# Optimization experiments

Measured on AMD Instinct MI355X. Metric: run time of the kernel, lower is better.

Reference implementation:

```python
import jax, jax.numpy as jnp
import numpy as np

B, S, C = 4, 2048, 768
H = 6
D = C // H  # head_dim = 128


def setup_inputs() -> dict:
    key = jax.random.key(0)
    k_x, k_wa, k_ba, k_wp, k_bp = jax.random.split(key, 5)
    scale = 1.0 / np.sqrt(C)
    return {
        "x": jax.random.normal(k_x, (B, S, C), dtype=jnp.float32),
        "w_attn": jax.random.normal(k_wa, (C, 3 * C), dtype=jnp.float32) * scale,
        "b_attn": jax.random.normal(k_ba, (3 * C,), dtype=jnp.float32) * 0.02,
        "w_proj": jax.random.normal(k_wp, (C, C), dtype=jnp.float32) * scale,
        "b_proj": jax.random.normal(k_bp, (C,), dtype=jnp.float32) * 0.02,
    }


def reference(x, w_attn, b_attn, w_proj, b_proj):
    Bb, Ss, Cc = x.shape
    qkv = x @ w_attn + b_attn                      # [B,S,3C]
    q, k, v = jnp.split(qkv, 3, axis=-1)
    # [B,S,C] -> [B,H,S,D]
    q = q.reshape(Bb, Ss, H, D).transpose(0, 2, 1, 3)
    k = k.reshape(Bb, Ss, H, D).transpose(0, 2, 1, 3)
    v = v.reshape(Bb, Ss, H, D).transpose(0, 2, 1, 3)
    scores = jnp.einsum("bhsd,bhtd->bhst", q, k) / jnp.sqrt(jnp.float32(D))
    causal = jnp.tril(jnp.ones((Ss, Ss), dtype=bool))  # [S,S]
    scores = jnp.where(causal[None, None], scores, -jnp.inf)
    attn = jax.nn.softmax(scores, axis=-1)             # [B,H,S,S]
    out = jnp.einsum("bhst,bhtd->bhsd", attn, v)       # [B,H,S,D]
    out = out.transpose(0, 2, 1, 3).reshape(Bb, Ss, Cc)
    return out @ w_proj + b_proj
```

## Files before the change

kernel.cpp:

```cpp
#include <hip/hip_runtime.h>
#include <hip/hip_bf16.h>
#include <stdint.h>

#define SS 2048
#define CC 768
#define C3 2304
#define NITEMS (32 * 24)

typedef float f32x4 __attribute__((ext_vector_type(4)));
typedef short s16x8 __attribute__((ext_vector_type(8)));

__device__ __forceinline__ unsigned short f2bf(float f) {
  union { float f; unsigned int u; } v; v.f = f;
  unsigned int r = (v.u + 0x7FFFu + ((v.u >> 16) & 1u)) >> 16;
  return (unsigned short)r;
}

__device__ __forceinline__ s16x8 ld8(const unsigned short* p) {
  return *reinterpret_cast<const s16x8*>(p);
}

__device__ __forceinline__ unsigned int cvt_pk_bf16(float lo, float hi) {
  unsigned int r;
  asm("v_cvt_pk_bf16_f32 %0, %1, %2" : "=v"(r) : "v"(lo), "v"(hi));
  return r;
}

__device__ __forceinline__ void gload_lds16(const unsigned short* g, unsigned short* l) {
  __builtin_amdgcn_global_load_lds(
      (const __attribute__((address_space(1))) void*)g,
      (__attribute__((address_space(3))) void*)l, 16, 0, 0);
}

__global__ __launch_bounds__(256) void cast_bf16_kernel(
    const float* __restrict__ src, unsigned short* __restrict__ dst, int n4) {
  int i = blockIdx.x * 256 + threadIdx.x;
  if (i < n4) {
    float4 v = reinterpret_cast<const float4*>(src)[i];
    ushort4 o;
    o.x = f2bf(v.x); o.y = f2bf(v.y); o.z = f2bf(v.z); o.w = f2bf(v.w);
    reinterpret_cast<ushort4*>(dst)[i] = o;
  }
}

__global__ __launch_bounds__(256) void transpose_cast_kernel(
    const float* __restrict__ src, unsigned short* __restrict__ dst, int R, int C) {
  __shared__ float tile[32][33];
  int c0 = blockIdx.x * 32, r0 = blockIdx.y * 32;
  int tx = threadIdx.x & 31, ty = threadIdx.x >> 5;
  #pragma unroll
  for (int i = 0; i < 32; i += 8)
    tile[ty + i][tx] = src[(size_t)(r0 + ty + i) * C + c0 + tx];
  __syncthreads();
  #pragma unroll
  for (int i = 0; i < 32; i += 8)
    dst[(size_t)(c0 + ty + i) * R + r0 + tx] = f2bf(tile[tx][ty + i]);
}

__global__ __launch_bounds__(256) void vtrans_kernel(
    const unsigned short* __restrict__ qkv, unsigned short* __restrict__ vT) {
  __shared__ unsigned short t[64 * 128];
  const int tid = threadIdx.x;
  const int n0 = blockIdx.x * 64;
  const int bh = blockIdx.y;
  const int b = bh / 6, h = bh % 6;
  #pragma unroll
  for (int it = 0; it < 4; ++it) {
    int c = it * 256 + tid;
    int n = c >> 4, slot = c & 15;
    s16x8 v = ld8(qkv + (size_t)(b * SS + n0 + n) * C3 + 2 * CC + h * 128 + slot * 8);
    int ss = slot ^ ((n >> 3) & 7);
    *reinterpret_cast<s16x8*>(&t[n * 128 + ss * 8]) = v;
  }
  __syncthreads();
  #pragma unroll
  for (int it = 0; it < 4; ++it) {
    int c = it * 256 + tid;
    int d = c >> 3, n8 = (c & 7) * 8;
    s16x8 o;
    #pragma unroll
    for (int j = 0; j < 8; ++j) {
      int n = n8 + j;
      int sl = (d >> 3) ^ ((n >> 3) & 7);
      o[j] = (short)t[n * 128 + sl * 8 + (d & 7)];
    }
    *reinterpret_cast<s16x8*>(&vT[((size_t)bh * 128 + d) * SS + n0 + n8]) = o;
  }
}

template <int OUT_BF16>
__global__ __launch_bounds__(256) void gemm_lds_kernel(
    const unsigned short* __restrict__ A, const unsigned short* __restrict__ Bt,
    const float* __restrict__ bias, void* __restrict__ out, int M, int N, int K) {
  __shared__ unsigned short lA[2][128 * 32];
  __shared__ unsigned short lB[2][128 * 32];
  const int tid = threadIdx.x, lane = tid & 63, w = tid >> 6;
  const int nbx = gridDim.x;
  int bid = blockIdx.y * nbx + blockIdx.x;
  const int cpx = (nbx * gridDim.y) >> 3;
  bid = (bid & 7) * cpx + (bid >> 3);
  const int m0 = (bid / nbx) * 128, n0 = (bid % nbx) * 128;
  const int lm = lane & 15, lg = lane >> 4;
  const int wm = (w >> 1) * 64, wn = (w & 1) * 64;
  const int sr = lane >> 2;
  const int ssl = ((lane & 3) ^ ((sr >> 1) & 3)) * 8;
  int aOff[4], bOff[4];
  #pragma unroll
  for (int i = 0; i < 4; ++i) {
    int ra = wm + i * 16 + lm, rb = wn + i * 16 + lm;
    aOff[i] = ra * 32 + ((lg ^ ((ra >> 1) & 3)) * 8);
    bOff[i] = rb * 32 + ((lg ^ ((rb >> 1) & 3)) * 8);
  }
  f32x4 acc[4][4] = {};
  const int nt = K / 32;
  #pragma unroll 1
  for (int t = -1; t < nt; ++t) {
    if (t + 1 < nt) {
      const int k0 = (t + 1) * 32;
      const int cs = (t + 1) & 1;
      #pragma unroll
      for (int i = 0; i < 2; ++i) {
        int c = w * 2 + i;
        int row = c * 16 + sr;
        gload_lds16(A + (size_t)(m0 + row) * K + k0 + ssl, &lA[cs][c * 512]);
        gload_lds16(Bt + (size_t)(n0 + row) * K + k0 + ssl, &lB[cs][c * 512]);
      }
    }
    if (t >= 0) {
      const int cu = t & 1;
      s16x8 af[4], bf[4];
      #pragma unroll
      for (int i = 0; i < 4; ++i) af[i] = ld8(&lA[cu][aOff[i]]);
      #pragma unroll
      for (int i = 0; i < 4; ++i) bf[i] = ld8(&lB[cu][bOff[i]]);
      __builtin_amdgcn_s_setprio(1);
      #pragma unroll
      for (int mi = 0; mi < 4; ++mi)
        #pragma unroll
        for (int ni = 0; ni < 4; ++ni)
          acc[mi][ni] = __builtin_amdgcn_mfma_f32_16x16x32_bf16(af[mi], bf[ni], acc[mi][ni], 0, 0, 0);
      __builtin_amdgcn_s_setprio(0);
    }
    __syncthreads();
  }
  #pragma unroll
  for (int mi = 0; mi < 4; ++mi) {
    #pragma unroll
    for (int ni = 0; ni < 4; ++ni) {
      const int row = m0 + wm + mi * 16 + lg * 4;
      const int col = n0 + wn + ni * 16 + lm;
      const float bs = bias[col];
      #pragma unroll
      for (int r = 0; r < 4; ++r) {
        float v = acc[mi][ni][r] + bs;
        if (OUT_BF16)
          ((unsigned short*)out)[(size_t)(row + r) * N + col] = f2bf(v);
        else
          ((float*)out)[(size_t)(row + r) * N + col] = v;
      }
    }
  }
}

__global__ __launch_bounds__(256) void attn_kernel(
    const unsigned short* __restrict__ qkv,
    const unsigned short* __restrict__ vT,
    unsigned short* __restrict__ aout,
    int* __restrict__ ctr) {
  const int tid = threadIdx.x, lane = tid & 63, w = tid >> 6;
  const int lm = lane & 15, lg = lane >> 4;
  __shared__ unsigned short kbuf[2][64 * 128];
  __shared__ unsigned short vbuf[2][128 * 64];
  __shared__ unsigned int pb[4][16 * 44];
  __shared__ int s_item;
  const float scale = 0.08838834764831845f;
  unsigned int* pr = &pb[w][lm * 44];
  const int klg4 = lane >> 4, ks16 = lane & 15;
  const int vlg8 = lane >> 3, vs8 = lane & 7;
  for (;;) {
    __syncthreads();
    if (tid == 0) s_item = atomicAdd(ctr, 1);
    __syncthreads();
    const int item = s_item;
    if (item >= NITEMS) return;
    const int qt = 31 - (item / 24);
    const int bh = item % 24;
    const int b = bh / 6, h = bh % 6;
    const int q0 = qt * 64, wq0 = q0 + w * 16;
    const unsigned short* base = qkv + (size_t)b * SS * C3;
    const unsigned short* kg = base + CC + h * 128;
    const unsigned short* vg = vT + (size_t)bh * 128 * SS;
    s16x8 qf[4];
    {
      const unsigned short* qp = base + (size_t)(wq0 + lm) * C3 + h * 128 + lg * 8;
      #pragma unroll
      for (int ks = 0; ks < 4; ++ks) qf[ks] = ld8(qp + ks * 32);
    }
    f32x4 oacc[8] = {};
    float m_run = -1e30f, l_run = 0.0f;
    const int nt = qt + 1;
    #pragma unroll 1
    for (int t = -1; t < nt; ++t) {
      if (t + 1 < nt) {
        const int n1 = (t + 1) * 64;
        const int cs = (t + 1) & 1;
        #pragma unroll
        for (int i = 0; i < 4; ++i) {
          int c = w * 4 + i;
          int r = c * 4 + klg4;
          gload_lds16(kg + (size_t)(n1 + r) * C3 + ((ks16 ^ (r & 7)) * 8),
                      &kbuf[cs][c * 512]);
        }
        #pragma unroll
        for (int i = 0; i < 4; ++i) {
          int c = w * 4 + i;
          int d = c * 8 + vlg8;
          gload_lds16(vg + (size_t)d * SS + n1 + ((vs8 ^ vlg8) * 8),
                      &vbuf[cs][c * 512]);
        }
      }
      if (t >= 0) {
        const int n0 = t * 64;
        const int cu = t & 1;
        const unsigned short* kb = kbuf[cu];
        const unsigned short* vb = vbuf[cu];
        f32x4 sacc[4] = {};
        __builtin_amdgcn_s_setprio(1);
        #pragma unroll
        for (int nsub = 0; nsub < 4; ++nsub) {
          const int kr = (nsub * 16 + lm) * 128;
          #pragma unroll
          for (int ks = 0; ks < 4; ++ks) {
            s16x8 kf = ld8(&kb[kr + (((ks * 4 + lg) ^ (lm & 7)) * 8)]);
            sacc[nsub] = __builtin_amdgcn_mfma_f32_16x16x32_bf16(kf, qf[ks], sacc[nsub], 0, 0, 0);
          }
        }
        __builtin_amdgcn_s_setprio(0);
        const int qg = wq0 + lm;
        const bool full = (n0 + 63 <= wq0);
        float xs[4][4];
        float tmax = -1e30f;
        #pragma unroll
        for (int nsub = 0; nsub < 4; ++nsub) {
          #pragma unroll
          for (int r = 0; r < 4; ++r) {
            int n = n0 + nsub * 16 + lg * 4 + r;
            float x = sacc[nsub][r] * scale;
            if (!full && n > qg) x = -1e30f;
            xs[nsub][r] = x;
            tmax = fmaxf(tmax, x);
          }
        }
        tmax = fmaxf(tmax, __shfl_xor(tmax, 16));
        tmax = fmaxf(tmax, __shfl_xor(tmax, 32));
        const bool noresc = __all(tmax - m_run <= 8.0f);
        const float m_new = noresc ? m_run : fmaxf(m_run, tmax);
        float psum = 0.0f;
        unsigned int pk_[4][2];
        #pragma unroll
        for (int nsub = 0; nsub < 4; ++nsub) {
          float p0 = __expf(xs[nsub][0] - m_new);
          float p1 = __expf(xs[nsub][1] - m_new);
          float p2 = __expf(xs[nsub][2] - m_new);
          float p3 = __expf(xs[nsub][3] - m_new);
          psum += (p0 + p1) + (p2 + p3);
          pk_[nsub][0] = cvt_pk_bf16(p0, p1);
          pk_[nsub][1] = cvt_pk_bf16(p2, p3);
        }
        psum += __shfl_xor(psum, 16);
        psum += __shfl_xor(psum, 32);
        if (!noresc) {
          const float resc = __expf(m_run - m_new);
          l_run *= resc;
          m_run = m_new;
          float rs[4];
          #pragma unroll
          for (int r = 0; r < 4; ++r) rs[r] = __shfl(resc, lg * 4 + r);
          #pragma unroll
          for (int dsub = 0; dsub < 8; ++dsub)
            #pragma unroll
            for (int r = 0; r < 4; ++r) oacc[dsub][r] *= rs[r];
        }
        l_run += psum;
        #pragma unroll
        for (int nsub = 0; nsub < 4; ++nsub) {
          uint2 pk2; pk2.x = pk_[nsub][0]; pk2.y = pk_[nsub][1];
          *reinterpret_cast<uint2*>(&pr[nsub * 8 + lg * 2]) = pk2;
        }
        __builtin_amdgcn_s_setprio(1);
        #pragma unroll
        for (int nch = 0; nch < 2; ++nch) {
          s16x8 pf = *reinterpret_cast<const s16x8*>(&pr[nch * 16 + lg * 4]);
          #pragma unroll
          for (int dsub = 0; dsub < 8; ++dsub) {
            const int vr = (dsub * 16 + lm) * 64;
            s16x8 vf = ld8(&vb[vr + (((nch * 4 + lg) ^ (lm & 7)) * 8)]);
            oacc[dsub] = __builtin_amdgcn_mfma_f32_16x16x32_bf16(pf, vf, oacc[dsub], 0, 0, 0);
          }
        }
        __builtin_amdgcn_s_setprio(0);
      }
      __syncthreads();
    }
    float linv[4];
    #pragma unroll
    for (int r = 0; r < 4; ++r) linv[r] = 1.0f / __shfl(l_run, lg * 4 + r);
    #pragma unroll
    for (int dsub = 0; dsub < 8; ++dsub) {
      const int col = h * 128 + dsub * 16 + lm;
      #pragma unroll
      for (int r = 0; r < 4; ++r)
        aout[(size_t)(b * SS + wq0 + lg * 4 + r) * CC + col] =
            f2bf(oacc[dsub][r] * linv[r]);
    }
  }
}

extern "C" void kernel_launch(void* const* d_in, const int* in_sizes, int n_in,
                              void* d_out, int out_size, void* d_ws, size_t ws_size,
                              hipStream_t stream) {
  const float* x      = (const float*)d_in[0];
  const float* w_attn = (const float*)d_in[1];
  const float* b_attn = (const float*)d_in[2];
  const float* w_proj = (const float*)d_in[3];
  const float* b_proj = (const float*)d_in[4];
  float* out = (float*)d_out;

  const size_t M = 4 * (size_t)SS;
  unsigned short* ws = (unsigned short*)d_ws;
  unsigned short* xb   = ws;
  unsigned short* waT  = xb + M * CC;
  unsigned short* wpT  = waT + (size_t)C3 * CC;
  unsigned short* qkv  = wpT + (size_t)CC * CC;
  unsigned short* aout = qkv + M * C3;
  unsigned short* vT   = xb;
  int* ctr = (int*)(aout + M * CC);

  int n4 = (int)(M * CC / 4);
  cast_bf16_kernel<<<(n4 + 255) / 256, 256, 0, stream>>>(x, xb, n4);
  transpose_cast_kernel<<<dim3(C3 / 32, CC / 32), 256, 0, stream>>>(w_attn, waT, CC, C3);
  transpose_cast_kernel<<<dim3(CC / 32, CC / 32), 256, 0, stream>>>(w_proj, wpT, CC, CC);

  gemm_lds_kernel<1><<<dim3(C3 / 128, M / 128), 256, 0, stream>>>(
      xb, waT, b_attn, (void*)qkv, (int)M, C3, CC);

  vtrans_kernel<<<dim3(SS / 64, 24), 256, 0, stream>>>(qkv, vT);

  hipMemsetAsync(ctr, 0, sizeof(int), stream);
  attn_kernel<<<512, 256, 0, stream>>>(qkv, vT, aout, ctr);

  gemm_lds_kernel<0><<<dim3(CC / 128, M / 128), 256, 0, stream>>>(
      aout, wpT, b_proj, (void*)out, (int)M, CC, CC);
}
```

Before: 195.4 us.

## Use partial vmcnt waits so next-stage loads overlap compute in GEMM and attention

Restructures the double-buffered loops in both the GEMM and attention kernels. The first stage is now issued before the loop. Each iteration issues the next stage's global-to-LDS loads and then waits only for the older group with s_waitcnt vmcnt(N), followed by an explicit barrier. Before, __syncthreads at the end of each iteration drained every outstanding load, including the prefetch just issued, so prefetch could not overlap compute. The change depends on hand-counted vmcnt values matching the number of loads issued per stage; a wrong count would be a correctness hazard.

```diff
diff --git a/kernel.cpp b/kernel.cpp
--- a/kernel.cpp
+++ b/kernel.cpp
@@ -113,35 +113,44 @@
   }
   f32x4 acc[4][4] = {};
   const int nt = K / 32;
+  #define GSTAGE(tt, bb)                                                      \
+    {                                                                         \
+      const int k0_ = (tt) * 32;                                              \
+      _Pragma("unroll")                                                       \
+      for (int i_ = 0; i_ < 2; ++i_) {                                        \
+        int c_ = w * 2 + i_;                                                  \
+        int row_ = c_ * 16 + sr;                                              \
+        gload_lds16(A + (size_t)(m0 + row_) * K + k0_ + ssl, &lA[bb][c_ * 512]); \
+        gload_lds16(Bt + (size_t)(n0 + row_) * K + k0_ + ssl, &lB[bb][c_ * 512]); \
+      }                                                                       \
+    }
+  GSTAGE(0, 0);
   #pragma unroll 1
-  for (int t = -1; t < nt; ++t) {
+  for (int t = 0; t < nt; ++t) {
     if (t + 1 < nt) {
-      const int k0 = (t + 1) * 32;
-      const int cs = (t + 1) & 1;
-      #pragma unroll
-      for (int i = 0; i < 2; ++i) {
-        int c = w * 2 + i;
-        int row = c * 16 + sr;
-        gload_lds16(A + (size_t)(m0 + row) * K + k0 + ssl, &lA[cs][c * 512]);
-        gload_lds16(Bt + (size_t)(n0 + row) * K + k0 + ssl, &lB[cs][c * 512]);
-      }
-    }
-    if (t >= 0) {
-      const int cu = t & 1;
-      s16x8 af[4], bf[4];
-      #pragma unroll
-      for (int i = 0; i < 4; ++i) af[i] = ld8(&lA[cu][aOff[i]]);
-      #pragma unroll
-      for (int i = 0; i < 4; ++i) bf[i] = ld8(&lB[cu][bOff[i]]);
-      __builtin_amdgcn_s_setprio(1);
-      #pragma unroll
-      for (int mi = 0; mi < 4; ++mi)
-        #pragma unroll
-        for (int ni = 0; ni < 4; ++ni)
-          acc[mi][ni] = __builtin_amdgcn_mfma_f32_16x16x32_bf16(af[mi], bf[ni], acc[mi][ni], 0, 0, 0);
-      __builtin_amdgcn_s_setprio(0);
-    }
-    __syncthreads();
+      GSTAGE(t + 1, (t + 1) & 1);
+      asm volatile("s_waitcnt vmcnt(4)" ::: "memory");
+    } else {
+      asm volatile("s_waitcnt vmcnt(0)" ::: "memory");
+    }
+    __builtin_amdgcn_sched_barrier(0);
+    __builtin_amdgcn_s_barrier();
+    const int cu = t & 1;
+    s16x8 af[4], bf[4];
+    #pragma unroll
+    for (int i = 0; i < 4; ++i) af[i] = ld8(&lA[cu][aOff[i]]);
+    #pragma unroll
+    for (int i = 0; i < 4; ++i) bf[i] = ld8(&lB[cu][bOff[i]]);
+    __builtin_amdgcn_s_setprio(1);
+    #pragma unroll
+    for (int mi = 0; mi < 4; ++mi)
+      #pragma unroll
+      for (int ni = 0; ni < 4; ++ni)
+        acc[mi][ni] = __builtin_amdgcn_mfma_f32_16x16x32_bf16(af[mi], bf[ni], acc[mi][ni], 0, 0, 0);
+    __builtin_amdgcn_s_setprio(0);
+    asm volatile("s_waitcnt lgkmcnt(0)" ::: "memory");
+    __builtin_amdgcn_sched_barrier(0);
+    __builtin_amdgcn_s_barrier();
   }
   #pragma unroll
   for (int mi = 0; mi < 4; ++mi) {
@@ -160,6 +169,7 @@
       }
     }
   }
+  #undef GSTAGE
 }
 
 __global__ __launch_bounds__(256) void attn_kernel(
@@ -196,112 +206,122 @@
       #pragma unroll
       for (int ks = 0; ks < 4; ++ks) qf[ks] = ld8(qp + ks * 32);
     }
+    #define ASTAGE(tt, bb)                                                    \
+      {                                                                       \
+        const int n1_ = (tt) * 64;                                            \
+        _Pragma("unroll")                                                     \
+        for (int i_ = 0; i_ < 4; ++i_) {                                      \
+          int c_ = w * 4 + i_;                                                \
+          int r_ = c_ * 4 + klg4;                                             \
+          gload_lds16(kg + (size_t)(n1_ + r_) * C3 + ((ks16 ^ (r_ & 7)) * 8), \
+                      &kbuf[bb][c_ * 512]);                                   \
+        }                                                                     \
+        _Pragma("unroll")                                                     \
+        for (int i_ = 0; i_ < 4; ++i_) {                                      \
+          int c_ = w * 4 + i_;                                                \
+          int d_ = c_ * 8 + vlg8;                                             \
+          gload_lds16(vg + (size_t)d_ * SS + n1_ + ((vs8 ^ vlg8) * 8),        \
+                      &vbuf[bb][c_ * 512]);                                   \
+        }                                                                     \
+      }
     f32x4 oacc[8] = {};
     float m_run = -1e30f, l_run = 0.0f;
     const int nt = qt + 1;
+    ASTAGE(0, 0);
     #pragma unroll 1
-    for (int t = -1; t < nt; ++t) {
+    for (int t = 0; t < nt; ++t) {
       if (t + 1 < nt) {
-        const int n1 = (t + 1) * 64;
-        const int cs = (t + 1) & 1;
-        #pragma unroll
-        for (int i = 0; i < 4; ++i) {
-          int c = w * 4 + i;
-          int r = c * 4 + klg4;
-          gload_lds16(kg + (size_t)(n1 + r) * C3 + ((ks16 ^ (r & 7)) * 8),
-                      &kbuf[cs][c * 512]);
+        ASTAGE(t + 1, (t + 1) & 1);
+        asm volatile("s_waitcnt vmcnt(8)" ::: "memory");
+      } else {
+        asm volatile("s_waitcnt vmcnt(0)" ::: "memory");
+      }
+      __builtin_amdgcn_sched_barrier(0);
+      __builtin_amdgcn_s_barrier();
+      const int n0 = t * 64;
+      const int cu = t & 1;
+      const unsigned short* kb = kbuf[cu];
+      const unsigned short* vb = vbuf[cu];
+      f32x4 sacc[4] = {};
+      __builtin_amdgcn_s_setprio(1);
+      #pragma unroll
+      for (int nsub = 0; nsub < 4; ++nsub) {
+        const int kr = (nsub * 16 + lm) * 128;
+        #pragma unroll
+        for (int ks = 0; ks < 4; ++ks) {
+          s16x8 kf = ld8(&kb[kr + (((ks * 4 + lg) ^ (lm & 7)) * 8)]);
+          sacc[nsub] = __builtin_amdgcn_mfma_f32_16x16x32_bf16(kf, qf[ks], sacc[nsub], 0, 0, 0);
         }
-        #pragma unroll
-        for (int i = 0; i < 4; ++i) {
-          int c = w * 4 + i;
-          int d = c * 8 + vlg8;
-          gload_lds16(vg + (size_t)d * SS + n1 + ((vs8 ^ vlg8) * 8),
-                      &vbuf[cs][c * 512]);
+      }
+      __builtin_amdgcn_s_setprio(0);
+      const int qg = wq0 + lm;
+      const bool full = (n0 + 63 <= wq0);
+      float xs[4][4];
+      float tmax = -1e30f;
+      #pragma unroll
+      for (int nsub = 0; nsub < 4; ++nsub) {
+        #pragma unroll
+        for (int r = 0; r < 4; ++r) {
+          int n = n0 + nsub * 16 + lg * 4 + r;
+          float x = sacc[nsub][r] * scale;
+          if (!full && n > qg) x = -1e30f;
+          xs[nsub][r] = x;
+          tmax = fmaxf(tmax, x);
         }
       }
-      if (t >= 0) {
-        const int n0 = t * 64;
-        const int cu = t & 1;
-        const unsigned short* kb = kbuf[cu];
-        const unsigned short* vb = vbuf[cu];
-        f32x4 sacc[4] = {};
-        __builtin_amdgcn_s_setprio(1);
-        #pragma unroll
-        for (int nsub = 0; nsub < 4; ++nsub) {
-          const int kr = (nsub * 16 + lm) * 128;
+      tmax = fmaxf(tmax, __shfl_xor(tmax, 16));
+      tmax = fmaxf(tmax, __shfl_xor(tmax, 32));
+      const bool noresc = __all(tmax - m_run <= 8.0f);
+      const float m_new = noresc ? m_run : fmaxf(m_run, tmax);
+      float psum = 0.0f;
+      unsigned int pk_[4][2];
+      #pragma unroll
+      for (int nsub = 0; nsub < 4; ++nsub) {
+        float p0 = __expf(xs[nsub][0] - m_new);
+        float p1 = __expf(xs[nsub][1] - m_new);
+        float p2 = __expf(xs[nsub][2] - m_new);
+        float p3 = __expf(xs[nsub][3] - m_new);
+        psum += (p0 + p1) + (p2 + p3);
+        pk_[nsub][0] = cvt_pk_bf16(p0, p1);
+        pk_[nsub][1] = cvt_pk_bf16(p2, p3);
+      }
+      psum += __shfl_xor(psum, 16);
+      psum += __shfl_xor(psum, 32);
+      if (!noresc) {
+        const float resc = __expf(m_run - m_new);
+        l_run *= resc;
+        m_run = m_new;
+        float rs[4];
+        #pragma unroll
+        for (int r = 0; r < 4; ++r) rs[r] = __shfl(resc, lg * 4 + r);
+        #pragma unroll
+        for (int dsub = 0; dsub < 8; ++dsub)
           #pragma unroll
-          for (int ks = 0; ks < 4; ++ks) {
-            s16x8 kf = ld8(&kb[kr + (((ks * 4 + lg) ^ (lm & 7)) * 8)]);
-            sacc[nsub] = __builtin_amdgcn_mfma_f32_16x16x32_bf16(kf, qf[ks], sacc[nsub], 0, 0, 0);
-          }
+          for (int r = 0; r < 4; ++r) oacc[dsub][r] *= rs[r];
+      }
+      l_run += psum;
+      #pragma unroll
+      for (int nsub = 0; nsub < 4; ++nsub) {
+        uint2 pk2; pk2.x = pk_[nsub][0]; pk2.y = pk_[nsub][1];
+        *reinterpret_cast<uint2*>(&pr[nsub * 8 + lg * 2]) = pk2;
+      }
+      __builtin_amdgcn_s_setprio(1);
+      #pragma unroll
+      for (int nch = 0; nch < 2; ++nch) {
+        s16x8 pf = *reinterpret_cast<const s16x8*>(&pr[nch * 16 + lg * 4]);
+        #pragma unroll
+        for (int dsub = 0; dsub < 8; ++dsub) {
+          const int vr = (dsub * 16 + lm) * 64;
+          s16x8 vf = ld8(&vb[vr + (((nch * 4 + lg) ^ (lm & 7)) * 8)]);
+          oacc[dsub] = __builtin_amdgcn_mfma_f32_16x16x32_bf16(pf, vf, oacc[dsub], 0, 0, 0);
         }
-        __builtin_amdgcn_s_setprio(0);
-        const int qg = wq0 + lm;
-        const bool full = (n0 + 63 <= wq0);
-        float xs[4][4];
-        float tmax = -1e30f;
-        #pragma unroll
-        for (int nsub = 0; nsub < 4; ++nsub) {
-          #pragma unroll
-          for (int r = 0; r < 4; ++r) {
-            int n = n0 + nsub * 16 + lg * 4 + r;
-            float x = sacc[nsub][r] * scale;
-            if (!full && n > qg) x = -1e30f;
-            xs[nsub][r] = x;
-            tmax = fmaxf(tmax, x);
-          }
-        }
-        tmax = fmaxf(tmax, __shfl_xor(tmax, 16));
-        tmax = fmaxf(tmax, __shfl_xor(tmax, 32));
-        const bool noresc = __all(tmax - m_run <= 8.0f);
-        const float m_new = noresc ? m_run : fmaxf(m_run, tmax);
-        float psum = 0.0f;
-        unsigned int pk_[4][2];
-        #pragma unroll
-        for (int nsub = 0; nsub < 4; ++nsub) {
-          float p0 = __expf(xs[nsub][0] - m_new);
-          float p1 = __expf(xs[nsub][1] - m_new);
-          float p2 = __expf(xs[nsub][2] - m_new);
-          float p3 = __expf(xs[nsub][3] - m_new);
-          psum += (p0 + p1) + (p2 + p3);
-          pk_[nsub][0] = cvt_pk_bf16(p0, p1);
-          pk_[nsub][1] = cvt_pk_bf16(p2, p3);
-        }
-        psum += __shfl_xor(psum, 16);
-        psum += __shfl_xor(psum, 32);
-        if (!noresc) {
-          const float resc = __expf(m_run - m_new);
-          l_run *= resc;
-          m_run = m_new;
-          float rs[4];
-          #pragma unroll
-          for (int r = 0; r < 4; ++r) rs[r] = __shfl(resc, lg * 4 + r);
-          #pragma unroll
-          for (int dsub = 0; dsub < 8; ++dsub)
-            #pragma unroll
-            for (int r = 0; r < 4; ++r) oacc[dsub][r] *= rs[r];
-        }
-        l_run += psum;
-        #pragma unroll
-        for (int nsub = 0; nsub < 4; ++nsub) {
-          uint2 pk2; pk2.x = pk_[nsub][0]; pk2.y = pk_[nsub][1];
-          *reinterpret_cast<uint2*>(&pr[nsub * 8 + lg * 2]) = pk2;
-        }
-        __builtin_amdgcn_s_setprio(1);
-        #pragma unroll
-        for (int nch = 0; nch < 2; ++nch) {
-          s16x8 pf = *reinterpret_cast<const s16x8*>(&pr[nch * 16 + lg * 4]);
-          #pragma unroll
-          for (int dsub = 0; dsub < 8; ++dsub) {
-            const int vr = (dsub * 16 + lm) * 64;
-            s16x8 vf = ld8(&vb[vr + (((nch * 4 + lg) ^ (lm & 7)) * 8)]);
-            oacc[dsub] = __builtin_amdgcn_mfma_f32_16x16x32_bf16(pf, vf, oacc[dsub], 0, 0, 0);
-          }
-        }
-        __builtin_amdgcn_s_setprio(0);
-      }
-      __syncthreads();
-    }
+      }
+      __builtin_amdgcn_s_setprio(0);
+      asm volatile("s_waitcnt lgkmcnt(0)" ::: "memory");
+      __builtin_amdgcn_sched_barrier(0);
+      __builtin_amdgcn_s_barrier();
+    }
+    #undef ASTAGE
     float linv[4];
     #pragma unroll
     for (int r = 0; r < 4; ++r) linv[r] = 1.0f / __shfl(l_run, lg * 4 + r);
```

Result: faster. 158.1 us (-19.1%).
